# Kernel optimization log

Hardware: AMD Instinct MI355X
Metric: run time of the kernel (lower is better)

Reference implementation:

```python
import jax, jax.numpy as jnp
import numpy as np

N = 100_000          # nodes
E = 3_200_000        # edges
DIM = 64             # filt_conv_dimension
L = 3                # filt_conv_number
MAX_DEG = 64         # embedding table size = MAX_DEG + 1
SUM_DIMS = DIM * (L + 1)  # 256, fc input
BN_EPS = 1e-5
NEG_SLOPE = 0.01


def _leaky(x):
    return jnp.where(x >= 0, x, NEG_SLOPE * x)


def _batchnorm(x, g, b):
    # training-mode BN over the node axis
    mu = jnp.mean(x, axis=0, keepdims=True)
    var = jnp.var(x, axis=0, keepdims=True)
    return g * (x - mu) * jax.lax.rsqrt(var + BN_EPS) + b


def setup_inputs() -> dict:
    key = jax.random.key(0)
    ks = jax.random.split(key, 16)
    s = 0.05
    inp = {
        "node_deg": jax.random.randint(ks[0], (N,), 0, MAX_DEG, dtype=jnp.int32),
        "edge_index": jax.random.randint(ks[1], (2, E), 0, N, dtype=jnp.int32),
        "embed_deg": jax.random.normal(ks[2], (MAX_DEG + 1, DIM), jnp.float32) * s,
        "eps": jnp.zeros((L,), jnp.float32),
        "W1": jax.random.normal(ks[3], (L, DIM, DIM), jnp.float32) * s,
        "b1": jnp.zeros((L, DIM), jnp.float32),
        "W2": jax.random.normal(ks[4], (L, DIM, DIM), jnp.float32) * s,
        "b2": jnp.zeros((L, DIM), jnp.float32),
        "bn_g": jnp.ones((L, DIM), jnp.float32),
        "bn_b": jnp.zeros((L, DIM), jnp.float32),
        "fc_W1": jax.random.normal(ks[5], (SUM_DIMS, DIM), jnp.float32) * s,
        "fc_b1": jnp.zeros((DIM,), jnp.float32),
        "fc_bn_g": jnp.ones((DIM,), jnp.float32),
        "fc_bn_b": jnp.zeros((DIM,), jnp.float32),
        "fc_W2": jax.random.normal(ks[6], (DIM, 1), jnp.float32) * s,
        "fc_b2": jnp.zeros((1,), jnp.float32),
    }
    return inp


def reference(node_deg, edge_index, embed_deg, eps, W1, b1, W2, b2,
              bn_g, bn_b, fc_W1, fc_b1, fc_bn_g, fc_bn_b, fc_W2, fc_b2):
    src, dst = edge_index[0], edge_index[1]
    h = embed_deg[node_deg]                       # [N, DIM]
    z = [h]
    for l in range(L):
        x = z[-1]
        # GINConv: (1+eps)*x_i + sum_{j->i} x_j, then MLP lin_lrelu_lin
        agg = jax.ops.segment_sum(x[src], dst, num_segments=N)  # [N, DIM]
        m = (1.0 + eps[l]) * x + agg
        h1 = _leaky(m @ W1[l] + b1[l])
        out = h1 @ W2[l] + b2[l]
        out = _leaky(_batchnorm(out, bn_g[l], bn_b[l]))
        z.append(out)
    xcat = jnp.concatenate(z, axis=1)             # [N, SUM_DIMS]
    hfc = _leaky(_batchnorm(xcat @ fc_W1 + fc_b1, fc_bn_g, fc_bn_b))
    ret = jax.nn.sigmoid(hfc @ fc_W2 + fc_b2)     # [N, 1]
    return jnp.squeeze(ret, axis=-1)              # [N]
```

## Files before the change

kernel.cpp:

```cpp
#include <hip/hip_runtime.h>
#include <hip/hip_bf16.h>

#define NN 100000
#define NE 3200000
#define D 64
#define BN_EPS 1e-5f

#define NP 512
#define CHUNK 6250
#define NB 391
#define SPREAD 16

typedef float v2f __attribute__((ext_vector_type(2)));

#define FMA4(accr, xs, w4) \
  accr.x += (xs) * (w4).x; accr.y += (xs) * (w4).y; \
  accr.z += (xs) * (w4).z; accr.w += (xs) * (w4).w;

__global__ __launch_bounds__(256) void precompute_kernel(
    const float* __restrict__ emb, const float* __restrict__ W1_0,
    const float* __restrict__ fcW1, float* __restrict__ E1,
    float* __restrict__ T) {
  __shared__ float A[64][64];
  __shared__ float B[64][64];
  int t = threadIdx.x;
  const float* W = (blockIdx.x == 0) ? W1_0 : fcW1;
  float* O = (blockIdx.x == 0) ? E1 : T;
  int wr = t >> 4, wc = (t & 15) * 4;
  #pragma unroll
  for (int j = 0; j < 4; j++) {
    *(float4*)&A[wr + 16 * j][wc] = *(const float4*)&emb[(long)(wr + 16 * j) * D + wc];
    *(float4*)&B[wr + 16 * j][wc] = *(const float4*)&W[(long)(wr + 16 * j) * D + wc];
  }
  __syncthreads();
  int c0 = (t & 15) * 4, r0 = (t >> 4) * 4;
  float4 acc[4];
  #pragma unroll
  for (int r = 0; r < 4; r++) acc[r] = make_float4(0.f, 0.f, 0.f, 0.f);
  for (int k = 0; k < 64; k++) {
    float4 w4 = *(const float4*)&B[k][c0];
    FMA4(acc[0], A[r0 + 0][k], w4); FMA4(acc[1], A[r0 + 1][k], w4);
    FMA4(acc[2], A[r0 + 2][k], w4); FMA4(acc[3], A[r0 + 3][k], w4);
  }
  #pragma unroll
  for (int r = 0; r < 4; r++)
    *(float4*)&O[(long)(r0 + r) * D + c0] = acc[r];
}

__global__ __launch_bounds__(256) void bucket_kernel(const int* __restrict__ ei,
    const int* __restrict__ deg, int* __restrict__ rec, int* __restrict__ S) {
  __shared__ int cntL[392];
  __shared__ int curL[392];
  __shared__ int scanbuf[256];
  int t = threadIdx.x;
  int p = blockIdx.x;
  int e0 = p * CHUNK;
  cntL[t] = 0;
  if (t < 136) cntL[256 + t] = 0;
  __syncthreads();
  {
    int e = t;
    for (; e + 768 < CHUNK; e += 1024) {
      int d0 = ei[NE + e0 + e];
      int d1 = ei[NE + e0 + e + 256];
      int d2 = ei[NE + e0 + e + 512];
      int d3 = ei[NE + e0 + e + 768];
      atomicAdd(&cntL[(unsigned)d0 >> 8], 1);
      atomicAdd(&cntL[(unsigned)d1 >> 8], 1);
      atomicAdd(&cntL[(unsigned)d2 >> 8], 1);
      atomicAdd(&cntL[(unsigned)d3 >> 8], 1);
    }
    for (; e < CHUNK; e += 256) {
      int dd = ei[NE + e0 + e];
      atomicAdd(&cntL[(unsigned)dd >> 8], 1);
    }
  }
  __syncthreads();
  int a0 = 0, a1 = 0;
  if (t < 196) { a0 = cntL[2 * t]; a1 = cntL[2 * t + 1]; }
  int s = a0 + a1;
  scanbuf[t] = s;
  __syncthreads();
  for (int off = 1; off < 256; off <<= 1) {
    int x = (t >= off) ? scanbuf[t - off] : 0;
    __syncthreads();
    scanbuf[t] += x;
    __syncthreads();
  }
  int ex = scanbuf[t] - s;
  if (t < 196) {
    curL[2 * t]     = ex;
    curL[2 * t + 1] = ex + a0;
    S[p * 392 + 2 * t]     = e0 + ex;
    S[p * 392 + 2 * t + 1] = e0 + ex + a0;
  }
  __syncthreads();
  {
    int e = t;
    for (; e + 768 < CHUNK; e += 1024) {
      int s0 = ei[e0 + e],       d0 = ei[NE + e0 + e];
      int s1 = ei[e0 + e + 256], d1 = ei[NE + e0 + e + 256];
      int s2 = ei[e0 + e + 512], d2 = ei[NE + e0 + e + 512];
      int s3 = ei[e0 + e + 768], d3 = ei[NE + e0 + e + 768];
      int g0 = deg[s0], g1 = deg[s1], g2 = deg[s2], g3 = deg[s3];
      int p0 = atomicAdd(&curL[(unsigned)d0 >> 8], 1);
      int p1 = atomicAdd(&curL[(unsigned)d1 >> 8], 1);
      int p2 = atomicAdd(&curL[(unsigned)d2 >> 8], 1);
      int p3 = atomicAdd(&curL[(unsigned)d3 >> 8], 1);
      rec[e0 + p0] = s0 | ((d0 & 255) << 17) | (g0 << 25);
      rec[e0 + p1] = s1 | ((d1 & 255) << 17) | (g1 << 25);
      rec[e0 + p2] = s2 | ((d2 & 255) << 17) | (g2 << 25);
      rec[e0 + p3] = s3 | ((d3 & 255) << 17) | (g3 << 25);
    }
    for (; e < CHUNK; e += 256) {
      int ss = ei[e0 + e];
      int dd = ei[NE + e0 + e];
      int dg = deg[ss];
      int b = (unsigned)dd >> 8;
      int pos = atomicAdd(&curL[b], 1);
      rec[e0 + pos] = ss | ((dd & 255) << 17) | (dg << 25);
    }
  }
}

__global__ __launch_bounds__(256) void bucketsum_kernel(const int* __restrict__ S,
    int* __restrict__ bsum) {
  __shared__ int sh[256];
  int B = blockIdx.x;
  int t = threadIdx.x;
  int c = 0;
  for (int p = t; p < NP; p += 256)
    c += S[p * 392 + B + 1] - S[p * 392 + B];
  sh[t] = c;
  __syncthreads();
  for (int o = 128; o > 0; o >>= 1) {
    if (t < o) sh[t] += sh[t + o];
    __syncthreads();
  }
  if (t == 0) bsum[B] = sh[0];
}

__global__ __launch_bounds__(512) void scan2_kernel(int* __restrict__ bsum) {
  __shared__ int sh[512];
  int t = threadIdx.x;
  int v = (t < NB) ? bsum[t] : 0;
  sh[t] = v;
  __syncthreads();
  for (int o = 1; o < 512; o <<= 1) {
    int x = (t >= o) ? sh[t - o] : 0;
    __syncthreads();
    sh[t] += x;
    __syncthreads();
  }
  if (t < NB) bsum[t] = sh[t] - v;
}

__global__ __launch_bounds__(512) void sort_kernel(const int* __restrict__ rec,
    const int* __restrict__ S, const int* __restrict__ bsum,
    int* __restrict__ csroff, int* __restrict__ csrsrc,
    unsigned* __restrict__ cnt8) {
  __shared__ int cntL[256];
  __shared__ int curL[256];
  __shared__ unsigned hist[256 * 33];
  int t = threadIdx.x;
  int B = blockIdx.x;
  if (t < 256) cntL[t] = 0;
  for (int k = t; k < 256 * 33; k += 512) hist[k] = 0;
  __syncthreads();
  int lane = t & 15;
  int g = t >> 4;
  for (int p = g; p < NP; p += 32) {
    int s0 = S[p * 392 + B], s1 = S[p * 392 + B + 1];
    for (int e = s0 + lane; e < s1; e += 16) {
      int r = rec[e];
      int dl = (r >> 17) & 255;
      int dg = (unsigned)r >> 25;
      atomicAdd(&cntL[dl], 1);
      atomicAdd(&hist[dl * 33 + (dg >> 1)], (dg & 1) ? 0x10000u : 1u);
    }
  }
  __syncthreads();
  int v = 0;
  if (t < 256) { v = cntL[t]; curL[t] = v; }
  __syncthreads();
  for (int o = 1; o < 256; o <<= 1) {
    int x = 0;
    if (t < 256 && t >= o) x = curL[t - o];
    __syncthreads();
    if (t < 256) curL[t] += x;
    __syncthreads();
  }
  int b0 = bsum[B];
  if (t < 256) {
    int excl = curL[t] - v;
    int node = B * 256 + t;
    if (node <= NN) csroff[node] = b0 + excl;
  }
  __syncthreads();
  if (t < 256) curL[t] = b0 + (curL[t] - v);
  if (t < 256) {
    int node = B * 256 + t;
    if (node < NN) {
      #pragma unroll
      for (int j = 0; j < 16; j++) {
        unsigned p0 = hist[t * 33 + 2 * j];
        unsigned p1 = hist[t * 33 + 2 * j + 1];
        unsigned p = (p0 & 255) | (((p0 >> 16) & 255) << 8)
                   | ((p1 & 255) << 16) | (((p1 >> 16) & 255) << 24);
        cnt8[(long)node * 16 + j] = p;
      }
    }
  }
  __syncthreads();
  for (int p = g; p < NP; p += 32) {
    int s0 = S[p * 392 + B], s1 = S[p * 392 + B + 1];
    for (int e = s0 + lane; e < s1; e += 16) {
      int r = rec[e];
      int pos = atomicAdd(&curL[(r >> 17) & 255], 1);
      csrsrc[pos] = r & 0x1FFFF;
    }
  }
}

__global__ __launch_bounds__(256) void agg_kernel(const int* __restrict__ off,
    const int* __restrict__ srcs, const unsigned* __restrict__ xh32,
    float* __restrict__ agg) {
  int t = threadIdx.x;
  int lane = t & 15;
  int g = t >> 4;
  int i = blockIdx.x * 16 + g;
  int e0 = off[i], e1 = off[i + 1];
  float s0 = 0.f, s1 = 0.f, s2 = 0.f, s3 = 0.f;
  int e = e0;
  for (; e + 8 <= e1; e += 8) {
    int j0 = srcs[e + 0], j1 = srcs[e + 1], j2 = srcs[e + 2], j3 = srcs[e + 3];
    int j4 = srcs[e + 4], j5 = srcs[e + 5], j6 = srcs[e + 6], j7 = srcs[e + 7];
    unsigned u0 = xh32[(long)j0 * 16 + lane];
    unsigned u1 = xh32[(long)j1 * 16 + lane];
    unsigned u2 = xh32[(long)j2 * 16 + lane];
    unsigned u3 = xh32[(long)j3 * 16 + lane];
    unsigned u4 = xh32[(long)j4 * 16 + lane];
    unsigned u5 = xh32[(long)j5 * 16 + lane];
    unsigned u6 = xh32[(long)j6 * 16 + lane];
    unsigned u7 = xh32[(long)j7 * 16 + lane];
    {
      v2f l0 = __builtin_amdgcn_cvt_pk_f32_fp8((int)u0, false);
      v2f h0 = __builtin_amdgcn_cvt_pk_f32_fp8((int)u0, true);
      v2f l1 = __builtin_amdgcn_cvt_pk_f32_fp8((int)u1, false);
      v2f h1 = __builtin_amdgcn_cvt_pk_f32_fp8((int)u1, true);
      v2f l2 = __builtin_amdgcn_cvt_pk_f32_fp8((int)u2, false);
      v2f h2 = __builtin_amdgcn_cvt_pk_f32_fp8((int)u2, true);
      v2f l3 = __builtin_amdgcn_cvt_pk_f32_fp8((int)u3, false);
      v2f h3 = __builtin_amdgcn_cvt_pk_f32_fp8((int)u3, true);
      s0 += (l0.x + l1.x) + (l2.x + l3.x);
      s1 += (l0.y + l1.y) + (l2.y + l3.y);
      s2 += (h0.x + h1.x) + (h2.x + h3.x);
      s3 += (h0.y + h1.y) + (h2.y + h3.y);
    }
    {
      v2f l0 = __builtin_amdgcn_cvt_pk_f32_fp8((int)u4, false);
      v2f h0 = __builtin_amdgcn_cvt_pk_f32_fp8((int)u4, true);
      v2f l1 = __builtin_amdgcn_cvt_pk_f32_fp8((int)u5, false);
      v2f h1 = __builtin_amdgcn_cvt_pk_f32_fp8((int)u5, true);
      v2f l2 = __builtin_amdgcn_cvt_pk_f32_fp8((int)u6, false);
      v2f h2 = __builtin_amdgcn_cvt_pk_f32_fp8((int)u6, true);
      v2f l3 = __builtin_amdgcn_cvt_pk_f32_fp8((int)u7, false);
      v2f h3 = __builtin_amdgcn_cvt_pk_f32_fp8((int)u7, true);
      s0 += (l0.x + l1.x) + (l2.x + l3.x);
      s1 += (l0.y + l1.y) + (l2.y + l3.y);
      s2 += (h0.x + h1.x) + (h2.x + h3.x);
      s3 += (h0.y + h1.y) + (h2.y + h3.y);
    }
  }
  for (; e + 4 <= e1; e += 4) {
    int j0 = srcs[e + 0], j1 = srcs[e + 1], j2 = srcs[e + 2], j3 = srcs[e + 3];
    unsigned u0 = xh32[(long)j0 * 16 + lane];
    unsigned u1 = xh32[(long)j1 * 16 + lane];
    unsigned u2 = xh32[(long)j2 * 16 + lane];
    unsigned u3 = xh32[(long)j3 * 16 + lane];
    v2f l0 = __builtin_amdgcn_cvt_pk_f32_fp8((int)u0, false);
    v2f h0 = __builtin_amdgcn_cvt_pk_f32_fp8((int)u0, true);
    v2f l1 = __builtin_amdgcn_cvt_pk_f32_fp8((int)u1, false);
    v2f h1 = __builtin_amdgcn_cvt_pk_f32_fp8((int)u1, true);
    v2f l2 = __builtin_amdgcn_cvt_pk_f32_fp8((int)u2, false);
    v2f h2 = __builtin_amdgcn_cvt_pk_f32_fp8((int)u2, true);
    v2f l3 = __builtin_amdgcn_cvt_pk_f32_fp8((int)u3, false);
    v2f h3 = __builtin_amdgcn_cvt_pk_f32_fp8((int)u3, true);
    s0 += (l0.x + l1.x) + (l2.x + l3.x);
    s1 += (l0.y + l1.y) + (l2.y + l3.y);
    s2 += (h0.x + h1.x) + (h2.x + h3.x);
    s3 += (h0.y + h1.y) + (h2.y + h3.y);
  }
  for (; e < e1; e++) {
    unsigned u = xh32[(long)srcs[e] * 16 + lane];
    v2f lo = __builtin_amdgcn_cvt_pk_f32_fp8((int)u, false);
    v2f hi = __builtin_amdgcn_cvt_pk_f32_fp8((int)u, true);
    s0 += lo.x; s1 += lo.y; s2 += hi.x; s3 += hi.y;
  }
  *(float4*)&agg[(long)i * D + lane * 4] = make_float4(s0, s1, s2, s3);
}

__global__ __launch_bounds__(256) void layer_kernel(
    const float* __restrict__ X,
    const float* __restrict__ AGG,
    const unsigned* __restrict__ CNT8, const float* __restrict__ E1,
    const int* __restrict__ deg,
    const float* __restrict__ epsv, int l,
    const float* __restrict__ W1, const float* __restrict__ b1,
    const float* __restrict__ W2, const float* __restrict__ b2,
    float* __restrict__ Z, float* __restrict__ spread)
{
  __shared__ float Ws[64][64];
  __shared__ float XsT[64][64];
  int t = threadIdx.x;
  int i0 = blockIdx.x * 64;
  float alpha = 1.0f + epsv[l];
  int c0 = (t & 15) * 4;
  int r0 = (t >> 4) * 4;
  int wr = t >> 4;
  int wc = (t & 15) * 4;
  int row = t & 63;
  int gi_row = i0 + row;
  int gis_row = (gi_row < NN) ? gi_row : NN - 1;
  int kb = (t >> 6) * 16;

  float4 h[4];
  if (CNT8) {
    #pragma unroll
    for (int j = 0; j < 4; j++)
      *(float4*)&Ws[wr + 16 * j][wc] = *(const float4*)&E1[(long)(wr + 16 * j) * D + wc];
    #pragma unroll
    for (int j = 0; j < 4; j++) {
      unsigned u = CNT8[(long)gis_row * 16 + (kb >> 2) + j];
      int k = kb + 4 * j;
      XsT[k + 0][row] = (float)(u & 255);
      XsT[k + 1][row] = (float)((u >> 8) & 255);
      XsT[k + 2][row] = (float)((u >> 16) & 255);
      XsT[k + 3][row] = (float)(u >> 24);
    }
    __syncthreads();
    float4 acc[4];
    #pragma unroll
    for (int r = 0; r < 4; r++) acc[r] = make_float4(0.f, 0.f, 0.f, 0.f);
    #pragma unroll 8
    for (int k = 0; k < 64; k++) {
      float4 w4 = *(const float4*)&Ws[k][c0];
      float4 x4 = *(const float4*)&XsT[k][r0];
      FMA4(acc[0], x4.x, w4); FMA4(acc[1], x4.y, w4);
      FMA4(acc[2], x4.z, w4); FMA4(acc[3], x4.w, w4);
    }
    float4 b4 = *(const float4*)&b1[c0];
    #pragma unroll
    for (int r = 0; r < 4; r++) {
      int gi = i0 + r0 + r;
      int gis = (gi < NN) ? gi : NN - 1;
      int dg = deg[gis];
      float4 e4 = *(const float4*)&Ws[dg][c0];
      h[r].x = b4.x + alpha * e4.x + acc[r].x;
      h[r].y = b4.y + alpha * e4.y + acc[r].y;
      h[r].z = b4.z + alpha * e4.z + acc[r].z;
      h[r].w = b4.w + alpha * e4.w + acc[r].w;
    }
  } else {
    #pragma unroll
    for (int j = 0; j < 4; j++)
      *(float4*)&Ws[wr + 16 * j][wc] = *(const float4*)&W1[(long)(wr + 16 * j) * D + wc];
    #pragma unroll
    for (int j = 0; j < 4; j++) {
      int k = kb + 4 * j;
      float4 xv = *(const float4*)&X[(long)gis_row * 256 + k];
      float4 a4 = *(const float4*)&AGG[(long)gis_row * D + k];
      XsT[k + 0][row] = alpha * xv.x + a4.x;
      XsT[k + 1][row] = alpha * xv.y + a4.y;
      XsT[k + 2][row] = alpha * xv.z + a4.z;
      XsT[k + 3][row] = alpha * xv.w + a4.w;
    }
    __syncthreads();
    {
      float4 b4 = *(const float4*)&b1[c0];
      #pragma unroll
      for (int r = 0; r < 4; r++) h[r] = b4;
    }
    #pragma unroll 8
    for (int k = 0; k < 64; k++) {
      float4 w4 = *(const float4*)&Ws[k][c0];
      float4 x4 = *(const float4*)&XsT[k][r0];
      FMA4(h[0], x4.x, w4); FMA4(h[1], x4.y, w4);
      FMA4(h[2], x4.z, w4); FMA4(h[3], x4.w, w4);
    }
  }
  #pragma unroll
  for (int r = 0; r < 4; r++) {
    h[r].x = (h[r].x >= 0.0f) ? h[r].x : 0.01f * h[r].x;
    h[r].y = (h[r].y >= 0.0f) ? h[r].y : 0.01f * h[r].y;
    h[r].z = (h[r].z >= 0.0f) ? h[r].z : 0.01f * h[r].z;
    h[r].w = (h[r].w >= 0.0f) ? h[r].w : 0.01f * h[r].w;
  }
  __syncthreads();
  #pragma unroll
  for (int r = 0; r < 4; r++) {
    XsT[c0 + 0][r0 + r] = h[r].x;
    XsT[c0 + 1][r0 + r] = h[r].y;
    XsT[c0 + 2][r0 + r] = h[r].z;
    XsT[c0 + 3][r0 + r] = h[r].w;
  }
  #pragma unroll
  for (int j = 0; j < 4; j++)
    *(float4*)&Ws[wr + 16 * j][wc] = *(const float4*)&W2[(long)(wr + 16 * j) * D + wc];
  __syncthreads();

  float4 z[4];
  {
    float4 b4 = *(const float4*)&b2[c0];
    #pragma unroll
    for (int r = 0; r < 4; r++) z[r] = b4;
  }
  #pragma unroll 8
  for (int k = 0; k < 64; k++) {
    float4 w4 = *(const float4*)&Ws[k][c0];
    float4 x4 = *(const float4*)&XsT[k][r0];
    FMA4(z[0], x4.x, w4); FMA4(z[1], x4.y, w4);
    FMA4(z[2], x4.z, w4); FMA4(z[3], x4.w, w4);
  }
  #pragma unroll
  for (int r = 0; r < 4; r++) {
    int gi = i0 + r0 + r;
    if (gi < NN) *(float4*)&Z[(long)gi * 256 + c0] = z[r];
  }

  float s[4] = {0, 0, 0, 0}, sq[4] = {0, 0, 0, 0};
  #pragma unroll
  for (int r = 0; r < 4; r++) {
    if (i0 + r0 + r < NN) {
      s[0] += z[r].x; sq[0] += z[r].x * z[r].x;
      s[1] += z[r].y; sq[1] += z[r].y * z[r].y;
      s[2] += z[r].z; sq[2] += z[r].z * z[r].z;
      s[3] += z[r].w; sq[3] += z[r].w * z[r].w;
    }
  }
  __syncthreads();
  float* red = &XsT[0][0];
  int grp = t >> 4;
  #pragma unroll
  for (int j = 0; j < 4; j++) {
    red[grp * 64 + c0 + j] = s[j];
    red[1024 + grp * 64 + c0 + j] = sq[j];
  }
  __syncthreads();
  if (t < 64) {
    float a = 0.0f, b = 0.0f;
    #pragma unroll
    for (int g = 0; g < 16; g++) {
      a += red[g * 64 + t];
      b += red[1024 + g * 64 + t];
    }
    int slot = blockIdx.x & (SPREAD - 1);
    atomicAdd(&spread[slot * 128 + t], a);
    atomicAdd(&spread[slot * 128 + 64 + t], b);
  }
}

__global__ __launch_bounds__(256) void fc1_kernel(
    const float* __restrict__ X, const int* __restrict__ deg,
    const float* __restrict__ T,
    const float* __restrict__ W, const float* __restrict__ bias,
    float* __restrict__ Y, float* __restrict__ spread)
{
  __shared__ float Ws[64][64];
  __shared__ float XsT[64][64];
  int t = threadIdx.x;
  int i0 = blockIdx.x * 64;
  int c0 = (t & 15) * 4;
  int r0 = (t >> 4) * 4;
  int wr = t >> 4;
  int wc = (t & 15) * 4;

  float4 acc[4];
  {
    float4 b4 = *(const float4*)&bias[c0];
    #pragma unroll
    for (int r = 0; r < 4; r++) {
      int gi = i0 + r0 + r;
      int gis = (gi < NN) ? gi : NN - 1;
      int dg = deg[gis];
      float4 t4 = *(const float4*)&T[(long)dg * D + c0];
      acc[r].x = b4.x + t4.x;
      acc[r].y = b4.y + t4.y;
      acc[r].z = b4.z + t4.z;
      acc[r].w = b4.w + t4.w;
    }
  }
  for (int kc = 64; kc < 256; kc += 64) {
    __syncthreads();
    #pragma unroll
    for (int j = 0; j < 4; j++)
      *(float4*)&Ws[wr + 16 * j][wc] = *(const float4*)&W[(long)(kc + wr + 16 * j) * D + wc];
    {
      int row = t & 63;
      int gi = i0 + row;
      int gis = (gi < NN) ? gi : NN - 1;
      int kb = (t >> 6) * 16;
      #pragma unroll
      for (int j = 0; j < 4; j++) {
        int k = kb + 4 * j;
        float4 xv = *(const float4*)&X[(long)gis * 256 + kc + k];
        XsT[k + 0][row] = xv.x;
        XsT[k + 1][row] = xv.y;
        XsT[k + 2][row] = xv.z;
        XsT[k + 3][row] = xv.w;
      }
    }
    __syncthreads();
    #pragma unroll 8
    for (int k = 0; k < 64; k++) {
      float4 w4 = *(const float4*)&Ws[k][c0];
      float4 x4 = *(const float4*)&XsT[k][r0];
      FMA4(acc[0], x4.x, w4); FMA4(acc[1], x4.y, w4);
      FMA4(acc[2], x4.z, w4); FMA4(acc[3], x4.w, w4);
    }
  }
  #pragma unroll
  for (int r = 0; r < 4; r++) {
    int gi = i0 + r0 + r;
    if (gi < NN) *(float4*)&Y[(long)gi * D + c0] = acc[r];
  }
  float s[4] = {0, 0, 0, 0}, sq[4] = {0, 0, 0, 0};
  #pragma unroll
  for (int r = 0; r < 4; r++) {
    if (i0 + r0 + r < NN) {
      s[0] += acc[r].x; sq[0] += acc[r].x * acc[r].x;
      s[1] += acc[r].y; sq[1] += acc[r].y * acc[r].y;
      s[2] += acc[r].z; sq[2] += acc[r].z * acc[r].z;
      s[3] += acc[r].w; sq[3] += acc[r].w * acc[r].w;
    }
  }
  __syncthreads();
  float* red = &XsT[0][0];
  int grp = t >> 4;
  #pragma unroll
  for (int j = 0; j < 4; j++) {
    red[grp * 64 + c0 + j] = s[j];
    red[1024 + grp * 64 + c0 + j] = sq[j];
  }
  __syncthreads();
  if (t < 64) {
    float a = 0.0f, b = 0.0f;
    #pragma unroll
    for (int g = 0; g < 16; g++) {
      a += red[g * 64 + t];
      b += red[1024 + g * 64 + t];
    }
    int slot = blockIdx.x & (SPREAD - 1);
    atomicAdd(&spread[slot * 128 + t], a);
    atomicAdd(&spread[slot * 128 + 64 + t], b);
  }
}

__global__ __launch_bounds__(256) void bn_apply_kernel(float* __restrict__ Zs,
    const float* __restrict__ spread,
    const float* __restrict__ g, const float* __restrict__ b,
    unsigned short* __restrict__ Outh) {
  __shared__ float st[128];
  int t = threadIdx.x;
  if (t < 128) {
    float a = 0.0f;
    #pragma unroll
    for (int gg = 0; gg < SPREAD; gg++) a += spread[gg * 128 + t];
    st[t] = a;
  }
  __syncthreads();
  int idx = blockIdx.x * 256 + t;
  int i = idx >> 5, dp = (idx & 31) * 2;
  if (i >= NN) return;
  float invn = 1.0f / (float)NN;
  float v0, v1;
  {
    float mu = st[dp] * invn;
    float var = fmaxf(st[64 + dp] * invn - mu * mu, 0.0f);
    float sc = g[dp] * rsqrtf(var + BN_EPS);
    v0 = sc * (Zs[(long)i * 256 + dp] - mu) + b[dp];
    v0 = (v0 >= 0.0f) ? v0 : 0.01f * v0;
  }
  {
    float mu = st[dp + 1] * invn;
    float var = fmaxf(st[64 + dp + 1] * invn - mu * mu, 0.0f);
    float sc = g[dp + 1] * rsqrtf(var + BN_EPS);
    v1 = sc * (Zs[(long)i * 256 + dp + 1] - mu) + b[dp + 1];
    v1 = (v1 >= 0.0f) ? v1 : 0.01f * v1;
  }
  Zs[(long)i * 256 + dp]     = v0;
  Zs[(long)i * 256 + dp + 1] = v1;
  if (Outh) {
    int packed = __builtin_amdgcn_cvt_pk_fp8_f32(v0, v1, 0, false);
    Outh[(long)i * 32 + (dp >> 1)] = (unsigned short)packed;
  }
}

__global__ __launch_bounds__(256) void fc2bn_kernel(const float* __restrict__ H,
    const float* __restrict__ spread,
    const float* __restrict__ g, const float* __restrict__ b,
    const float* __restrict__ W2, const float* __restrict__ b2,
    float* __restrict__ out) {
  __shared__ float st[128];
  int tid = threadIdx.x;
  if (tid < 128) {
    float a = 0.0f;
    #pragma unroll
    for (int gg = 0; gg < SPREAD; gg++) a += spread[gg * 128 + tid];
    st[tid] = a;
  }
  __syncthreads();
  int k = tid & 63, q = tid >> 6;
  int i = blockIdx.x * 4 + q;
  float invn = 1.0f / (float)NN;
  float mu = st[k] * invn;
  float var = fmaxf(st[64 + k] * invn - mu * mu, 0.0f);
  float sc = g[k] * rsqrtf(var + BN_EPS);
  float v = 0.0f;
  if (i < NN) {
    float hv = sc * (H[(long)i * D + k] - mu) + b[k];
    hv = (hv >= 0.0f) ? hv : 0.01f * hv;
    v = hv * W2[k];
  }
  #pragma unroll
  for (int off = 32; off > 0; off >>= 1)
    v += __shfl_down(v, off);
  if (k == 0 && i < NN) {
    float x = v + b2[0];
    out[i] = 1.0f / (1.0f + __expf(-x));
  }
}

extern "C" void kernel_launch(void* const* d_in, const int* in_sizes, int n_in,
                              void* d_out, int out_size, void* d_ws, size_t ws_size,
                              hipStream_t stream) {
  const int*   node_deg   = (const int*)d_in[0];
  const int*   edge_index = (const int*)d_in[1];
  const float* embedw     = (const float*)d_in[2];
  const float* eps        = (const float*)d_in[3];
  const float* W1         = (const float*)d_in[4];
  const float* b1         = (const float*)d_in[5];
  const float* W2         = (const float*)d_in[6];
  const float* b2         = (const float*)d_in[7];
  const float* bn_g       = (const float*)d_in[8];
  const float* bn_b       = (const float*)d_in[9];
  const float* fc_W1      = (const float*)d_in[10];
  const float* fc_b1      = (const float*)d_in[11];
  const float* fc_bn_g    = (const float*)d_in[12];
  const float* fc_bn_b    = (const float*)d_in[13];
  const float* fc_W2      = (const float*)d_in[14];
  const float* fc_b2      = (const float*)d_in[15];

  float* zcat   = (float*)d_ws;
  float* agg    = zcat + (long)NN * 256;
  float* statsS = agg + (long)NN * D;
  float* statsF = statsS + 4 * SPREAD * 128;
  int*   csroff = (int*)(statsF + 512);
  int*   bsum   = csroff + NN + 1;
  int*   csrsrc = bsum + 512;
  int*   rec    = csrsrc + NE;
  int*   S      = rec + NE;
  unsigned* cnt8 = (unsigned*)(S + NP * 392);
  float* E1     = (float*)(cnt8 + (long)NN * 16);
  float* Tt     = E1 + 64 * 64;
  unsigned short* xh = (unsigned short*)rec;

  const int rowBlocks   = NN / 4;
  const int layerBlocks = (NN + 63) / 64;
  const int aggBlocks   = NN / 16;
  const int bnBlocks    = (NN * 32 + 255) / 256;

  precompute_kernel<<<2, 256, 0, stream>>>(embedw, W1, fc_W1, E1, Tt);
  bucket_kernel<<<NP, 256, 0, stream>>>(edge_index, node_deg, rec, S);
  bucketsum_kernel<<<NB, 256, 0, stream>>>(S, bsum);
  scan2_kernel<<<1, 512, 0, stream>>>(bsum);
  sort_kernel<<<NB, 512, 0, stream>>>(rec, S, bsum, csroff, csrsrc, cnt8);

  hipMemsetAsync(statsS, 0, (size_t)(4 * SPREAD * 128) * sizeof(float), stream);

  for (int l = 0; l < 3; ++l) {
    if (l > 0)
      agg_kernel<<<aggBlocks, 256, 0, stream>>>(csroff, csrsrc,
          (const unsigned*)xh, agg);
    layer_kernel<<<layerBlocks, 256, 0, stream>>>(zcat + l * D,
        (l == 0) ? nullptr : agg,
        (l == 0) ? cnt8 : nullptr, E1, node_deg,
        eps, l,
        W1 + (long)l * D * D, b1 + (long)l * D,
        W2 + (long)l * D * D, b2 + (long)l * D,
        zcat + (l + 1) * D, statsS + (long)l * SPREAD * 128);
    bn_apply_kernel<<<bnBlocks, 256, 0, stream>>>(zcat + (l + 1) * D,
        statsS + (long)l * SPREAD * 128,
        bn_g + (long)l * D, bn_b + (long)l * D,
        (l < 2) ? xh : nullptr);
  }

  fc1_kernel<<<layerBlocks, 256, 0, stream>>>(zcat, node_deg, Tt,
      fc_W1, fc_b1, agg, statsS + 3L * SPREAD * 128);
  fc2bn_kernel<<<rowBlocks, 256, 0, stream>>>(agg, statsS + 3L * SPREAD * 128,
      fc_bn_g, fc_bn_b, fc_W2, fc_b2, (float*)d_out);
}
```

Baseline: 478.6 us.

## Fuse batchnorm+leaky apply into consumer kernels instead of rewriting fp32 activations

The bn_apply kernel no longer writes normalized fp32 values back into zcat. It now only emits the fp8 copy used by aggregation. The consuming layer kernel and fc1 kernel reduce the spread stats into shared memory and apply batchnorm and leaky-relu on the fly when loading X. This removes a full read-modify-write pass over zcat per layer and the third bn_apply launch, at the cost of recomputing the normalization per load and an extra stats reduction per block.

```diff
diff --git a/kernel.cpp b/kernel.cpp
--- a/kernel.cpp
+++ b/kernel.cpp
@@ -16,6 +16,16 @@
 #define FMA4(accr, xs, w4) \
   accr.x += (xs) * (w4).x; accr.y += (xs) * (w4).y; \
   accr.z += (xs) * (w4).z; accr.w += (xs) * (w4).w;
+
+__device__ __forceinline__ float bn_leaky(float x, const float* st, int d,
+    const float* g, const float* b) {
+  float invn = 1.0f / (float)NN;
+  float mu = st[d] * invn;
+  float var = fmaxf(st[64 + d] * invn - mu * mu, 0.0f);
+  float sc = g[d] * rsqrtf(var + BN_EPS);
+  float v = sc * (x - mu) + b[d];
+  return (v >= 0.0f) ? v : 0.01f * v;
+}
 
 __global__ __launch_bounds__(256) void precompute_kernel(
     const float* __restrict__ emb, const float* __restrict__ W1_0,
@@ -305,6 +315,8 @@
     const float* __restrict__ AGG,
     const unsigned* __restrict__ CNT8, const float* __restrict__ E1,
     const int* __restrict__ deg,
+    const float* __restrict__ spreadPrev,
+    const float* __restrict__ gPrev, const float* __restrict__ bPrev,
     const float* __restrict__ epsv, int l,
     const float* __restrict__ W1, const float* __restrict__ b1,
     const float* __restrict__ W2, const float* __restrict__ b2,
@@ -312,6 +324,7 @@
 {
   __shared__ float Ws[64][64];
   __shared__ float XsT[64][64];
+  __shared__ float st[128];
   int t = threadIdx.x;
   int i0 = blockIdx.x * 64;
   float alpha = 1.0f + epsv[l];
@@ -362,18 +375,25 @@
       h[r].w = b4.w + alpha * e4.w + acc[r].w;
     }
   } else {
+    if (t < 128) {
+      float a = 0.0f;
+      #pragma unroll
+      for (int gg = 0; gg < SPREAD; gg++) a += spreadPrev[gg * 128 + t];
+      st[t] = a;
+    }
     #pragma unroll
     for (int j = 0; j < 4; j++)
       *(float4*)&Ws[wr + 16 * j][wc] = *(const float4*)&W1[(long)(wr + 16 * j) * D + wc];
+    __syncthreads();
     #pragma unroll
     for (int j = 0; j < 4; j++) {
       int k = kb + 4 * j;
       float4 xv = *(const float4*)&X[(long)gis_row * 256 + k];
       float4 a4 = *(const float4*)&AGG[(long)gis_row * D + k];
-      XsT[k + 0][row] = alpha * xv.x + a4.x;
-      XsT[k + 1][row] = alpha * xv.y + a4.y;
-      XsT[k + 2][row] = alpha * xv.z + a4.z;
-      XsT[k + 3][row] = alpha * xv.w + a4.w;
+      XsT[k + 0][row] = alpha * bn_leaky(xv.x, st, k + 0, gPrev, bPrev) + a4.x;
+      XsT[k + 1][row] = alpha * bn_leaky(xv.y, st, k + 1, gPrev, bPrev) + a4.y;
+      XsT[k + 2][row] = alpha * bn_leaky(xv.z, st, k + 2, gPrev, bPrev) + a4.z;
+      XsT[k + 3][row] = alpha * bn_leaky(xv.w, st, k + 3, gPrev, bPrev) + a4.w;
     }
     __syncthreads();
     {
@@ -462,18 +482,31 @@
 
 __global__ __launch_bounds__(256) void fc1_kernel(
     const float* __restrict__ X, const int* __restrict__ deg,
-    const float* __restrict__ T,
+    const float* __restrict__ T, const float* __restrict__ statsAll,
+    const float* __restrict__ bng, const float* __restrict__ bnb,
     const float* __restrict__ W, const float* __restrict__ bias,
     float* __restrict__ Y, float* __restrict__ spread)
 {
   __shared__ float Ws[64][64];
   __shared__ float XsT[64][64];
+  __shared__ float st3[384];
   int t = threadIdx.x;
   int i0 = blockIdx.x * 64;
   int c0 = (t & 15) * 4;
   int r0 = (t >> 4) * 4;
   int wr = t >> 4;
   int wc = (t & 15) * 4;
+
+  if (t < 128) {
+    #pragma unroll
+    for (int ss = 0; ss < 3; ss++) {
+      float a = 0.0f;
+      #pragma unroll
+      for (int gg = 0; gg < SPREAD; gg++)
+        a += statsAll[(long)ss * SPREAD * 128 + gg * 128 + t];
+      st3[ss * 128 + t] = a;
+    }
+  }
 
   float4 acc[4];
   {
@@ -491,6 +524,10 @@
     }
   }
   for (int kc = 64; kc < 256; kc += 64) {
+    int sidx = (kc >> 6) - 1;
+    const float* st = &st3[sidx * 128];
+    const float* g = bng + sidx * D;
+    const float* b = bnb + sidx * D;
     __syncthreads();
     #pragma unroll
     for (int j = 0; j < 4; j++)
@@ -504,10 +541,10 @@
       for (int j = 0; j < 4; j++) {
         int k = kb + 4 * j;
         float4 xv = *(const float4*)&X[(long)gis * 256 + kc + k];
-        XsT[k + 0][row] = xv.x;
-        XsT[k + 1][row] = xv.y;
-        XsT[k + 2][row] = xv.z;
-        XsT[k + 3][row] = xv.w;
+        XsT[k + 0][row] = bn_leaky(xv.x, st, k + 0, g, b);
+        XsT[k + 1][row] = bn_leaky(xv.y, st, k + 1, g, b);
+        XsT[k + 2][row] = bn_leaky(xv.z, st, k + 2, g, b);
+        XsT[k + 3][row] = bn_leaky(xv.w, st, k + 3, g, b);
       }
     }
     __syncthreads();
@@ -556,7 +593,7 @@
   }
 }
 
-__global__ __launch_bounds__(256) void bn_apply_kernel(float* __restrict__ Zs,
+__global__ __launch_bounds__(256) void bn_apply_kernel(const float* __restrict__ Zs,
     const float* __restrict__ spread,
     const float* __restrict__ g, const float* __restrict__ b,
     unsigned short* __restrict__ Outh) {
@@ -572,28 +609,10 @@
   int idx = blockIdx.x * 256 + t;
   int i = idx >> 5, dp = (idx & 31) * 2;
   if (i >= NN) return;
-  float invn = 1.0f / (float)NN;
-  float v0, v1;
-  {
-    float mu = st[dp] * invn;
-    float var = fmaxf(st[64 + dp] * invn - mu * mu, 0.0f);
-    float sc = g[dp] * rsqrtf(var + BN_EPS);
-    v0 = sc * (Zs[(long)i * 256 + dp] - mu) + b[dp];
-    v0 = (v0 >= 0.0f) ? v0 : 0.01f * v0;
-  }
-  {
-    float mu = st[dp + 1] * invn;
-    float var = fmaxf(st[64 + dp + 1] * invn - mu * mu, 0.0f);
-    float sc = g[dp + 1] * rsqrtf(var + BN_EPS);
-    v1 = sc * (Zs[(long)i * 256 + dp + 1] - mu) + b[dp + 1];
-    v1 = (v1 >= 0.0f) ? v1 : 0.01f * v1;
-  }
-  Zs[(long)i * 256 + dp]     = v0;
-  Zs[(long)i * 256 + dp + 1] = v1;
-  if (Outh) {
-    int packed = __builtin_amdgcn_cvt_pk_fp8_f32(v0, v1, 0, false);
-    Outh[(long)i * 32 + (dp >> 1)] = (unsigned short)packed;
-  }
+  float v0 = bn_leaky(Zs[(long)i * 256 + dp], st, dp, g, b);
+  float v1 = bn_leaky(Zs[(long)i * 256 + dp + 1], st, dp + 1, g, b);
+  int packed = __builtin_amdgcn_cvt_pk_fp8_f32(v0, v1, 0, false);
+  Outh[(long)i * 32 + (dp >> 1)] = (unsigned short)packed;
 }
 
 __global__ __launch_bounds__(256) void fc2bn_kernel(const float* __restrict__ H,
@@ -612,14 +631,9 @@
   __syncthreads();
   int k = tid & 63, q = tid >> 6;
   int i = blockIdx.x * 4 + q;
-  float invn = 1.0f / (float)NN;
-  float mu = st[k] * invn;
-  float var = fmaxf(st[64 + k] * invn - mu * mu, 0.0f);
-  float sc = g[k] * rsqrtf(var + BN_EPS);
   float v = 0.0f;
   if (i < NN) {
-    float hv = sc * (H[(long)i * D + k] - mu) + b[k];
-    hv = (hv >= 0.0f) ? hv : 0.01f * hv;
+    float hv = bn_leaky(H[(long)i * D + k], st, k, g, b);
     v = hv * W2[k];
   }
   #pragma unroll
@@ -685,18 +699,21 @@
     layer_kernel<<<layerBlocks, 256, 0, stream>>>(zcat + l * D,
         (l == 0) ? nullptr : agg,
         (l == 0) ? cnt8 : nullptr, E1, node_deg,
+        (l == 0) ? nullptr : statsS + (long)(l - 1) * SPREAD * 128,
+        (l == 0) ? nullptr : bn_g + (long)(l - 1) * D,
+        (l == 0) ? nullptr : bn_b + (long)(l - 1) * D,
         eps, l,
         W1 + (long)l * D * D, b1 + (long)l * D,
         W2 + (long)l * D * D, b2 + (long)l * D,
         zcat + (l + 1) * D, statsS + (long)l * SPREAD * 128);
-    bn_apply_kernel<<<bnBlocks, 256, 0, stream>>>(zcat + (l + 1) * D,
-        statsS + (long)l * SPREAD * 128,
-        bn_g + (long)l * D, bn_b + (long)l * D,
-        (l < 2) ? xh : nullptr);
+    if (l < 2)
+      bn_apply_kernel<<<bnBlocks, 256, 0, stream>>>(zcat + (l + 1) * D,
+          statsS + (long)l * SPREAD * 128,
+          bn_g + (long)l * D, bn_b + (long)l * D, xh);
   }
 
   fc1_kernel<<<layerBlocks, 256, 0, stream>>>(zcat, node_deg, Tt,
-      fc_W1, fc_b1, agg, statsS + 3L * SPREAD * 128);
+      statsS, bn_g, bn_b, fc_W1, fc_b1, agg, statsS + 3L * SPREAD * 128);
   fc2bn_kernel<<<rowBlocks, 256, 0, stream>>>(agg, statsS + 3L * SPREAD * 128,
       fc_bn_g, fc_bn_b, fc_W2, fc_b2, (float*)d_out);
 }
```

Measured after the change: 486.1 us. About the same (+1.6%).
